# Performance work log

Hardware: AMD Instinct MI355X
Metric: run time of the kernel (lower is better)

Reference implementation:

```python
import jax, jax.numpy as jnp
import numpy as np

B, N, T, D, H, K = 8, 100, 16, 4, 64, 2
E = N * (N - 1)  # 9900 directed edges (fully connected, no self-loops)


def setup_inputs() -> dict:
    key = jax.random.key(0)
    ks = jax.random.split(key, 12)
    inputs = jax.random.normal(ks[0], (B, N, T, D), jnp.float32)
    # edge-type distribution per directed pair (softmax over K types)
    rel_type = jax.nn.softmax(jax.random.normal(ks[1], (B, E, K), jnp.float32), axis=-1)
    # one-hot receiver / sender incidence matrices for fully-connected graph
    off = ~np.eye(N, dtype=bool)
    send_idx, rec_idx = np.where(off)
    eye = np.eye(N, dtype=np.float32)
    rel_rec = jnp.asarray(eye[rec_idx])    # [E, N]
    rel_send = jnp.asarray(eye[send_idx])  # [E, N]
    s = 0.1
    msg_fc1_w = jax.random.normal(ks[2], (K, H, 2 * D), jnp.float32) * s
    msg_fc1_b = jax.random.normal(ks[3], (K, H), jnp.float32) * s
    msg_fc2_w = jax.random.normal(ks[4], (K, H, H), jnp.float32) * s
    msg_fc2_b = jax.random.normal(ks[5], (K, H), jnp.float32) * s
    out_fc1_w = jax.random.normal(ks[6], (H, D + H), jnp.float32) * s
    out_fc1_b = jax.random.normal(ks[7], (H,), jnp.float32) * s
    out_fc2_w = jax.random.normal(ks[8], (H, H), jnp.float32) * s
    out_fc2_b = jax.random.normal(ks[9], (H,), jnp.float32) * s
    out_fc3_w = jax.random.normal(ks[10], (D, H), jnp.float32) * s
    out_fc3_b = jax.random.normal(ks[11], (D,), jnp.float32) * s
    return {
        "inputs": inputs, "rel_type": rel_type,
        "rel_rec": rel_rec, "rel_send": rel_send,
        "msg_fc1_w": msg_fc1_w, "msg_fc1_b": msg_fc1_b,
        "msg_fc2_w": msg_fc2_w, "msg_fc2_b": msg_fc2_b,
        "out_fc1_w": out_fc1_w, "out_fc1_b": out_fc1_b,
        "out_fc2_w": out_fc2_w, "out_fc2_b": out_fc2_b,
        "out_fc3_w": out_fc3_w, "out_fc3_b": out_fc3_b,
        "pred_steps": 1,
    }


def reference(inputs, rel_type, rel_rec, rel_send,
              msg_fc1_w, msg_fc1_b, msg_fc2_w, msg_fc2_b,
              out_fc1_w, out_fc1_b, out_fc2_w, out_fc2_b,
              out_fc3_w, out_fc3_b, pred_steps):
    # inputs: [B, N, T, D] -> [B, T, N, D]
    x = jnp.transpose(inputs, (0, 2, 1, 3))
    b, t, n, d = x.shape
    # rel_type: [B, E, K] -> [B, T, E, K]
    rt = jnp.broadcast_to(rel_type[:, None], (b, t, rel_type.shape[1], rel_type.shape[2]))

    def single_step(xs, rts):
        # gather endpoint states: [B, T', E, D]
        recv = jnp.einsum('en,btnd->bted', rel_rec, xs)
        send = jnp.einsum('en,btnd->bted', rel_send, xs)
        pre_msg = jnp.concatenate([send, recv], axis=-1)  # [B, T', E, 2D]
        # per-edge-type MLP, skipping edge type 0 (skip_first_edge_type=True)
        h1 = jax.nn.relu(jnp.einsum('btef,khf->btekh', pre_msg, msg_fc1_w[1:]) + msg_fc1_b[1:])
        h2 = jax.nn.relu(jnp.einsum('btekh,kgh->btekg', h1, msg_fc2_w[1:]) + msg_fc2_b[1:])
        # mask by edge-type weight and sum over types -> [B, T', E, H]
        all_msgs = jnp.einsum('btekh,btek->bteh', h2, rts[..., 1:])
        # aggregate messages at receivers: [B, T', N, H]
        agg = jnp.einsum('bteh,en->btnh', all_msgs, rel_rec)
        aug = jnp.concatenate([xs, agg], axis=-1)  # [B, T', N, D+H]
        p = jax.nn.relu(aug @ out_fc1_w.T + out_fc1_b)
        p = jax.nn.relu(p @ out_fc2_w.T + out_fc2_b)
        p = p @ out_fc3_w.T + out_fc3_b
        return xs + p

    last_pred = x[:, 0::pred_steps]
    curr_rt = rt[:, 0::pred_steps]
    preds = []
    for _ in range(pred_steps):
        last_pred = single_step(last_pred, curr_rt)
        preds.append(last_pred)
    tp = preds[0].shape[1]
    # interleave: output[:, i::pred_steps] = preds[i]
    output = jnp.stack(preds, axis=2).reshape(b, tp * pred_steps, n, d)
    pred_all = output[:, : t - 1]  # [B, T-1, N, D]
    return jnp.transpose(pred_all, (0, 2, 1, 3))  # [B, N, T-1, D]
```

## Files before the change

kernel.cpp:

```cpp
#include <hip/hip_runtime.h>
#include <hip/hip_fp16.h>

#define B_  8
#define N_  100
#define T_  16
#define TP_ 15
#define D_  4
#define H_  64
#define E_  9900
#define NG  25
#define ROWS 12000

#define WS_AIN 0u
#define WS_V   2304000u
#define WS_RTT 3840000u
#define WS_UBF 4198400u
#define WS_W2F 5928960u
#define WS_W1F 5937152u
#define WS_W2B 5949440u
#define WS_W3F 5957632u

typedef __attribute__((ext_vector_type(8))) _Float16 f16x8;
typedef __attribute__((ext_vector_type(4))) float f32x4;

__device__ __forceinline__ void gload_lds16(const void* g, void* lds) {
    __builtin_amdgcn_global_load_lds(
        (const __attribute__((address_space(1))) void*)g,
        (__attribute__((address_space(3))) void*)lds, 16, 0, 0);
}

__device__ __forceinline__ f16x8 relu_add8(uint4 u, uint4 v) {
    const f16x8 a = __builtin_bit_cast(f16x8, u);
    const f16x8 b = __builtin_bit_cast(f16x8, v);
    const f16x8 s = a + b;
    const f16x8 z = (f16x8)(_Float16)0;
    return __builtin_elementwise_max(s, z);
}

__global__ __launch_bounds__(256)
void nri_prep(const float* __restrict__ x, const float* __restrict__ rel,
              const float* __restrict__ w1, const float* __restrict__ b1,
              const float* __restrict__ w2, const float* __restrict__ f1w,
              const float* __restrict__ f2w, const float* __restrict__ f3w,
              __half* __restrict__ ubf, __half* __restrict__ v_h,
              float* __restrict__ rtt, __half* __restrict__ ain,
              __half* __restrict__ w2f, __half* __restrict__ w1f,
              __half* __restrict__ w2b, __half* __restrict__ w3f)
{
    const int lane = threadIdx.x & 63;
    const int wid  = blockIdx.x * 4 + (threadIdx.x >> 6);

    if (wid < ROWS) {
        const int nn = wid % N_;
        const int bt = wid / N_;
        const int t  = bt % TP_;
        const int b  = bt / TP_;
        const float4 ws4 = *(const float4*)(w1 + lane * 8);
        const float4 wr4 = *(const float4*)(w1 + lane * 8 + 4);
        const float4 xv  = *(const float4*)(x + (((size_t)b * N_ + nn) * T_ + t) * D_);
        const float u = ws4.x * xv.x + ws4.y * xv.y + ws4.z * xv.z + ws4.w * xv.w;
        const float v = wr4.x * xv.x + wr4.y * xv.y + wr4.z * xv.z + wr4.w * xv.w
                        + b1[lane];
        ubf[(size_t)bt * 7200 + nn * 72 + lane] = __float2half(u);
        v_h[(size_t)wid * 64 + lane] = __float2half(v);
        if (lane == 32) {
            const unsigned short h0 = __half_as_ushort(__float2half(xv.x));
            const unsigned short h1 = __half_as_ushort(__float2half(xv.y));
            const unsigned short h2 = __half_as_ushort(__float2half(xv.z));
            const unsigned short h3 = __half_as_ushort(__float2half(xv.w));
            uint2 p; p.x = (unsigned)h0 | ((unsigned)h1 << 16);
                     p.y = (unsigned)h2 | ((unsigned)h3 << 16);
            *(uint2*)(ain + (size_t)wid * 96 + 64) = p;
        } else if (lane >= 33 && lane < 40) {
            uint2 zz; zz.x = 0u; zz.y = 0u;
            *(uint2*)(ain + (size_t)wid * 96 + 68 + (lane - 33) * 4) = zz;
        }
    } else if (wid < ROWS + B_ * N_) {
        const int idx = wid - ROWS;
        const int n = idx % N_;
        const int b = idx / N_;
        float* dst = rtt + (size_t)idx * 112;
        const int ia  = lane + (lane >= n ? 1 : 0);
        const int eda = ia * (N_ - 1) + (n < ia ? n : n - 1);
        dst[lane] = rel[((size_t)b * E_ + eda) * 2 + 1];
        if (lane < 48) {
            const int e2 = 64 + lane;
            float rv = 0.f;
            if (e2 < N_ - 1) {
                const int ib  = e2 + (e2 >= n ? 1 : 0);
                const int edb = ib * (N_ - 1) + (n < ib ? n : n - 1);
                rv = rel[((size_t)b * E_ + edb) * 2 + 1];
            }
            dst[64 + lane] = rv;
        }
    } else {
        const int fid = wid - (ROWS + B_ * N_);
        const int g16 = lane & 15, q = lane >> 4;
        unsigned short h[8];
        if (fid < 8) {
            const int s = fid >> 2, nt = fid & 3;
            const int g = nt * 16 + g16;
            #pragma unroll
            for (int j = 0; j < 8; ++j)
                h[j] = __half_as_ushort(__float2half(
                    w2[(size_t)g * 64 + s * 32 + q * 8 + j]));
            uint4 pv; pv.x = h[0] | ((unsigned)h[1] << 16); pv.y = h[2] | ((unsigned)h[3] << 16);
                      pv.z = h[4] | ((unsigned)h[5] << 16); pv.w = h[6] | ((unsigned)h[7] << 16);
            *(uint4*)(w2f + fid * 512 + lane * 8) = pv;
        } else if (fid < 20) {
            const int f = fid - 8;
            const int s = f >> 2, nt = f & 3;
            const int g = nt * 16 + g16;
            #pragma unroll
            for (int j = 0; j < 8; ++j) {
                const int k = s * 32 + q * 8 + j;
                float v = 0.f;
                if (k < 64)       v = f1w[(size_t)g * 68 + 4 + k];
                else if (k < 68)  v = f1w[(size_t)g * 68 + (k - 64)];
                h[j] = __half_as_ushort(__float2half(v));
            }
            uint4 pv; pv.x = h[0] | ((unsigned)h[1] << 16); pv.y = h[2] | ((unsigned)h[3] << 16);
                      pv.z = h[4] | ((unsigned)h[5] << 16); pv.w = h[6] | ((unsigned)h[7] << 16);
            *(uint4*)(w1f + f * 512 + lane * 8) = pv;
        } else if (fid < 28) {
            const int f = fid - 20;
            const int s = f >> 2, nt = f & 3;
            const int g = nt * 16 + g16;
            #pragma unroll
            for (int j = 0; j < 8; ++j)
                h[j] = __half_as_ushort(__float2half(
                    f2w[(size_t)g * 64 + s * 32 + q * 8 + j]));
            uint4 pv; pv.x = h[0] | ((unsigned)h[1] << 16); pv.y = h[2] | ((unsigned)h[3] << 16);
                      pv.z = h[4] | ((unsigned)h[5] << 16); pv.w = h[6] | ((unsigned)h[7] << 16);
            *(uint4*)(w2b + f * 512 + lane * 8) = pv;
        } else if (fid == 28) {
            unsigned short hh[16];
            #pragma unroll
            for (int nt = 0; nt < 4; ++nt)
                #pragma unroll
                for (int d = 0; d < 4; ++d)
                    hh[nt * 4 + d] = __half_as_ushort(__float2half(
                        f3w[d * 64 + nt * 16 + g16]));
            uint4 p0, p1;
            p0.x = hh[0] | ((unsigned)hh[1] << 16);  p0.y = hh[2] | ((unsigned)hh[3] << 16);
            p0.z = hh[4] | ((unsigned)hh[5] << 16);  p0.w = hh[6] | ((unsigned)hh[7] << 16);
            p1.x = hh[8] | ((unsigned)hh[9] << 16);  p1.y = hh[10] | ((unsigned)hh[11] << 16);
            p1.z = hh[12] | ((unsigned)hh[13] << 16); p1.w = hh[14] | ((unsigned)hh[15] << 16);
            *(uint4*)(w3f + lane * 16) = p0;
            *(uint4*)(w3f + lane * 16 + 8) = p1;
        }
    }
}

__global__ __launch_bounds__(256)
void nri_agg(const __half* __restrict__ ubf, const __half* __restrict__ v_h,
             const float* __restrict__ rtt, const __half* __restrict__ w2f,
             const float* __restrict__ b2, __half* __restrict__ ain)
{
    __shared__ __half u_lds[7680];

    const int tid  = threadIdx.x;
    const int lane = tid & 63;
    const int w    = tid >> 6;
    const int bid  = blockIdx.x;
    const int g  = bid % NG;
    const int t  = (bid / NG) % TP_;
    const int b  = bid / (NG * TP_);
    const int bt = b * TP_ + t;

    {
        const char* gsrc = (const char*)(ubf + (size_t)bt * 7200);
        char* ldst = (char*)u_lds;
        #pragma unroll
        for (int j = 0; j < 4; ++j) {
            const int c = w + 4 * j;
            if (c < 15)
                gload_lds16(gsrc + c * 1024 + lane * 16, ldst + c * 1024);
        }
    }

    const int col = lane & 15;
    const int q   = lane >> 4;
    const int kq  = q * 8;

    f16x8 bfr[8];
    #pragma unroll
    for (int f = 0; f < 8; ++f)
        bfr[f] = *(const f16x8*)((const char*)w2f + f * 1024 + lane * 16);

    const int n   = g * 4 + w;
    const int row = bt * N_ + n;
    const __half* vp = v_h + (size_t)row * 64;
    const uint4 vv0 = *(const uint4*)(vp + kq);
    const uint4 vv1 = *(const uint4*)(vp + 32 + kq);
    float bb[4];
    #pragma unroll
    for (int nt = 0; nt < 4; ++nt) bb[nt] = b2[nt * 16 + col];
    const float* rtp = rtt + ((size_t)b * N_ + n) * 112 + q * 4;

    __syncthreads();

    float aggl[4] = {0.f, 0.f, 0.f, 0.f};
    #pragma unroll
    for (int mf = 0; mf < 7; ++mf) {
        const int e = mf * 16 + col;
        int i = e + (e >= n ? 1 : 0);
        if (i > N_ - 1) i = N_ - 1;
        const float4 rt4 = *(const float4*)(rtp + mf * 16);
        f32x4 acc[4] = {};
        const uint4 ud0 = *(const uint4*)&u_lds[i * 72 + kq];
        const f16x8 af0 = relu_add8(ud0, vv0);
        #pragma unroll
        for (int nt = 0; nt < 4; ++nt)
            acc[nt] = __builtin_amdgcn_mfma_f32_16x16x32_f16(af0, bfr[nt], acc[nt], 0, 0, 0);
        const uint4 ud1 = *(const uint4*)&u_lds[i * 72 + 32 + kq];
        const f16x8 af1 = relu_add8(ud1, vv1);
        #pragma unroll
        for (int nt = 0; nt < 4; ++nt)
            acc[nt] = __builtin_amdgcn_mfma_f32_16x16x32_f16(af1, bfr[4 + nt], acc[nt], 0, 0, 0);
        #pragma unroll
        for (int nt = 0; nt < 4; ++nt) {
            aggl[nt] += fmaxf(acc[nt][0] + bb[nt], 0.f) * rt4.x
                      + fmaxf(acc[nt][1] + bb[nt], 0.f) * rt4.y
                      + fmaxf(acc[nt][2] + bb[nt], 0.f) * rt4.z
                      + fmaxf(acc[nt][3] + bb[nt], 0.f) * rt4.w;
        }
    }
    #pragma unroll
    for (int nt = 0; nt < 4; ++nt) {
        float p = aggl[nt];
        p += __shfl_xor(p, 16, 64);
        p += __shfl_xor(p, 32, 64);
        if (lane < 16)
            ain[(size_t)row * 96 + nt * 16 + col] = __float2half(p);
    }
}

__global__ __launch_bounds__(256)
void nri_out(const __half* __restrict__ ain, const __half* __restrict__ w1f,
             const __half* __restrict__ w2b, const __half* __restrict__ w3f,
             const float* __restrict__ f1b, const float* __restrict__ f2b,
             const float* __restrict__ f3b, const float* __restrict__ x,
             float* __restrict__ out)
{
    __shared__ __half p1buf[4][16 * 72];

    const int tid  = threadIdx.x;
    const int lane = tid & 63;
    const int w    = tid >> 6;
    const int row0 = (blockIdx.x * 4 + w) * 16;
    if (row0 >= ROWS) return;

    const int col = lane & 15;
    const int q   = lane >> 4;
    const int kq  = q * 8;

    f16x8 w1r[12];
    #pragma unroll
    for (int f = 0; f < 12; ++f)
        w1r[f] = *(const f16x8*)((const char*)w1f + f * 1024 + lane * 16);
    f16x8 w2r[8];
    #pragma unroll
    for (int f = 0; f < 8; ++f)
        w2r[f] = *(const f16x8*)((const char*)w2b + f * 1024 + lane * 16);
    float b1v[4], b2v[4];
    #pragma unroll
    for (int nt = 0; nt < 4; ++nt) { b1v[nt] = f1b[nt * 16 + col]; b2v[nt] = f2b[nt * 16 + col]; }
    const float4 b3v = *(const float4*)f3b;
    float w3v[16];
    {
        const uint4 p0 = *(const uint4*)(w3f + col * 16);
        const uint4 p1 = *(const uint4*)(w3f + col * 16 + 8);
        const unsigned* pp0 = (const unsigned*)&p0;
        const unsigned* pp1 = (const unsigned*)&p1;
        #pragma unroll
        for (int i = 0; i < 4; ++i) {
            w3v[2*i]     = __half2float(__ushort_as_half((unsigned short)(pp0[i] & 0xffff)));
            w3v[2*i + 1] = __half2float(__ushort_as_half((unsigned short)(pp0[i] >> 16)));
            w3v[8 + 2*i]     = __half2float(__ushort_as_half((unsigned short)(pp1[i] & 0xffff)));
            w3v[8 + 2*i + 1] = __half2float(__ushort_as_half((unsigned short)(pp1[i] >> 16)));
        }
    }

    f32x4 acc1[4] = {};
    #pragma unroll
    for (int s = 0; s < 3; ++s) {
        const uint4 ad = *(const uint4*)(ain + (size_t)(row0 + col) * 96 + s * 32 + kq);
        const f16x8 af = __builtin_bit_cast(f16x8, ad);
        #pragma unroll
        for (int nt = 0; nt < 4; ++nt)
            acc1[nt] = __builtin_amdgcn_mfma_f32_16x16x32_f16(af, w1r[s * 4 + nt], acc1[nt], 0, 0, 0);
    }
    #pragma unroll
    for (int nt = 0; nt < 4; ++nt)
        #pragma unroll
        for (int j = 0; j < 4; ++j)
            p1buf[w][(q * 4 + j) * 72 + nt * 16 + col] =
                __float2half(fmaxf(acc1[nt][j] + b1v[nt], 0.f));
    asm volatile("s_waitcnt lgkmcnt(0)" ::: "memory");
    __builtin_amdgcn_wave_barrier();

    f32x4 acc2[4] = {};
    #pragma unroll
    for (int s = 0; s < 2; ++s) {
        const uint4 pd = *(const uint4*)&p1buf[w][col * 72 + s * 32 + kq];
        const f16x8 af = __builtin_bit_cast(f16x8, pd);
        #pragma unroll
        for (int nt = 0; nt < 4; ++nt)
            acc2[nt] = __builtin_amdgcn_mfma_f32_16x16x32_f16(af, w2r[s * 4 + nt], acc2[nt], 0, 0, 0);
    }
    float p2v[4][4];
    #pragma unroll
    for (int nt = 0; nt < 4; ++nt)
        #pragma unroll
        for (int j = 0; j < 4; ++j)
            p2v[nt][j] = fmaxf(acc2[nt][j] + b2v[nt], 0.f);

    float pr[4][4];
    #pragma unroll
    for (int d = 0; d < 4; ++d)
        #pragma unroll
        for (int j = 0; j < 4; ++j) {
            float s = w3v[0 * 4 + d] * p2v[0][j] + w3v[1 * 4 + d] * p2v[1][j]
                    + w3v[2 * 4 + d] * p2v[2][j] + w3v[3 * 4 + d] * p2v[3][j];
            s += __shfl_xor(s, 1, 64);
            s += __shfl_xor(s, 2, 64);
            s += __shfl_xor(s, 4, 64);
            s += __shfl_xor(s, 8, 64);
            pr[d][j] = s;
        }

    if (col == 0) {
        #pragma unroll
        for (int j = 0; j < 4; ++j) {
            const int rg = row0 + q * 4 + j;
            const int n  = rg % N_;
            const int bt = rg / N_;
            const int t  = bt % TP_;
            const int b  = bt / TP_;
            const float4 xv = *(const float4*)(x + (((size_t)b * N_ + n) * T_ + t) * D_);
            float4 o;
            o.x = xv.x + b3v.x + pr[0][j];
            o.y = xv.y + b3v.y + pr[1][j];
            o.z = xv.z + b3v.z + pr[2][j];
            o.w = xv.w + b3v.w + pr[3][j];
            *(float4*)(out + (((size_t)b * N_ + n) * TP_ + t) * D_) = o;
        }
    }
}

extern "C" void kernel_launch(void* const* d_in, const int* in_sizes, int n_in,
                              void* d_out, int out_size, void* d_ws, size_t ws_size,
                              hipStream_t stream) {
    const float* x   = (const float*)d_in[0];
    const float* rel = (const float*)d_in[1];
    const float* w1  = (const float*)d_in[4] + 1 * H_ * 2 * D_;
    const float* b1  = (const float*)d_in[5] + 1 * H_;
    const float* w2  = (const float*)d_in[6] + 1 * H_ * H_;
    const float* b2  = (const float*)d_in[7] + 1 * H_;
    const float* f1w = (const float*)d_in[8];
    const float* f1b = (const float*)d_in[9];
    const float* f2w = (const float*)d_in[10];
    const float* f2b = (const float*)d_in[11];
    const float* f3w = (const float*)d_in[12];
    const float* f3b = (const float*)d_in[13];
    float* out = (float*)d_out;

    unsigned char* ws = (unsigned char*)d_ws;
    __half* ain = (__half*)(ws + WS_AIN);
    __half* v_h = (__half*)(ws + WS_V);
    float*  rtt = (float*)(ws + WS_RTT);
    __half* ubf = (__half*)(ws + WS_UBF);
    __half* w2f = (__half*)(ws + WS_W2F);
    __half* w1f = (__half*)(ws + WS_W1F);
    __half* w2b = (__half*)(ws + WS_W2B);
    __half* w3f = (__half*)(ws + WS_W3F);

    nri_prep<<<dim3(3208), 256, 0, stream>>>(x, rel, w1, b1, w2, f1w, f2w, f3w,
                                             ubf, v_h, rtt, ain,
                                             w2f, w1f, w2b, w3f);
    nri_agg<<<dim3(B_ * TP_ * NG), 256, 0, stream>>>(ubf, v_h, rtt, w2f, b2, ain);
    nri_out<<<dim3((ROWS / 16 + 3) / 4), 256, 0, stream>>>(ain, w1f, w2b, w3f,
                                                           f1b, f2b, f3b, x, out);
}
```

Before: 39.57 us.

## Remap agg block indices, fold bias into MFMA accumulators, add setprio hints

The block index mapping in nri_agg now interleaves 8 consecutive (b,t) slices across adjacent block IDs, which changes how blocks spread over CUs and caches. The second-layer bias is preloaded into the MFMA accumulators instead of being added afterwards, and the epilogue uses chained fmaf. s_setprio raises wave priority around the MFMA bursts to improve interleaving with other waves. Together these aim to trim VALU work and improve scheduling, but the block remap assumes B*TP is divisible by 8 (120 is) and may change L2 locality.

Result: no change. 39.59 us (+0.0%).

```diff
diff --git a/kernel.cpp b/kernel.cpp
--- a/kernel.cpp
+++ b/kernel.cpp
@@ -163,19 +163,21 @@
     const int lane = tid & 63;
     const int w    = tid >> 6;
     const int bid  = blockIdx.x;
-    const int g  = bid % NG;
-    const int t  = (bid / NG) % TP_;
-    const int b  = bid / (NG * TP_);
-    const int bt = b * TP_ + t;
+    const int c   = bid & 7;
+    const int idx = bid >> 3;
+    const int btc = idx / NG;
+    const int g   = idx - btc * NG;
+    const int bt  = btc * 8 + c;
+    const int b   = bt / TP_;
 
     {
         const char* gsrc = (const char*)(ubf + (size_t)bt * 7200);
         char* ldst = (char*)u_lds;
         #pragma unroll
         for (int j = 0; j < 4; ++j) {
-            const int c = w + 4 * j;
-            if (c < 15)
-                gload_lds16(gsrc + c * 1024 + lane * 16, ldst + c * 1024);
+            const int cch = w + 4 * j;
+            if (cch < 15)
+                gload_lds16(gsrc + cch * 1024 + lane * 16, ldst + cch * 1024);
         }
     }
 
@@ -207,23 +209,32 @@
         int i = e + (e >= n ? 1 : 0);
         if (i > N_ - 1) i = N_ - 1;
         const float4 rt4 = *(const float4*)(rtp + mf * 16);
-        f32x4 acc[4] = {};
+        f32x4 acc[4];
+        #pragma unroll
+        for (int nt = 0; nt < 4; ++nt) {
+            acc[nt][0] = bb[nt]; acc[nt][1] = bb[nt];
+            acc[nt][2] = bb[nt]; acc[nt][3] = bb[nt];
+        }
         const uint4 ud0 = *(const uint4*)&u_lds[i * 72 + kq];
-        const f16x8 af0 = relu_add8(ud0, vv0);
+        f16x8 af = relu_add8(ud0, vv0);
+        __builtin_amdgcn_s_setprio(1);
         #pragma unroll
         for (int nt = 0; nt < 4; ++nt)
-            acc[nt] = __builtin_amdgcn_mfma_f32_16x16x32_f16(af0, bfr[nt], acc[nt], 0, 0, 0);
+            acc[nt] = __builtin_amdgcn_mfma_f32_16x16x32_f16(af, bfr[nt], acc[nt], 0, 0, 0);
+        __builtin_amdgcn_s_setprio(0);
         const uint4 ud1 = *(const uint4*)&u_lds[i * 72 + 32 + kq];
-        const f16x8 af1 = relu_add8(ud1, vv1);
+        af = relu_add8(ud1, vv1);
+        __builtin_amdgcn_s_setprio(1);
         #pragma unroll
         for (int nt = 0; nt < 4; ++nt)
-            acc[nt] = __builtin_amdgcn_mfma_f32_16x16x32_f16(af1, bfr[4 + nt], acc[nt], 0, 0, 0);
+            acc[nt] = __builtin_amdgcn_mfma_f32_16x16x32_f16(af, bfr[4 + nt], acc[nt], 0, 0, 0);
+        __builtin_amdgcn_s_setprio(0);
         #pragma unroll
         for (int nt = 0; nt < 4; ++nt) {
-            aggl[nt] += fmaxf(acc[nt][0] + bb[nt], 0.f) * rt4.x
-                      + fmaxf(acc[nt][1] + bb[nt], 0.f) * rt4.y
-                      + fmaxf(acc[nt][2] + bb[nt], 0.f) * rt4.z
-                      + fmaxf(acc[nt][3] + bb[nt], 0.f) * rt4.w;
+            aggl[nt] = fmaf(fmaxf(acc[nt][0], 0.f), rt4.x, aggl[nt]);
+            aggl[nt] = fmaf(fmaxf(acc[nt][1], 0.f), rt4.y, aggl[nt]);
+            aggl[nt] = fmaf(fmaxf(acc[nt][2], 0.f), rt4.z, aggl[nt]);
+            aggl[nt] = fmaf(fmaxf(acc[nt][3], 0.f), rt4.w, aggl[nt]);
         }
     }
     #pragma unroll
```
